# Kernel optimization log

Measured on AMD Instinct MI355X. Metric: run time of the kernel, lower is better.

## Reference

```python
import jax, jax.numpy as jnp
import numpy as np

CONF_THRESH = 0.01
TOP_K = 200        # per-class NMS candidate cap
NMS_THRESH = 0.45
KEEP_TOP_K = 200   # global per-image cap; also output K
TEMPERATURE = 1.0
V0, V1 = 0.1, 0.2  # variances


def _nms_keep(bxs, scs):
    """Greedy NMS over candidates sorted descending by score.
    bxs: [M,4] (x1,y1,x2,y2), scs: [M] (invalid slots have score -1).
    Returns keep mask [M] (bool). Matches torch nm_suppression: a box j is
    suppressed by kept box i iff NOT (IoU(i,j) <= thresh) (NaN IoU suppresses)."""
    x1, y1, x2, y2 = bxs[:, 0], bxs[:, 1], bxs[:, 2], bxs[:, 3]
    area = (x2 - x1) * (y2 - y1)
    xx1 = jnp.maximum(x1[:, None], x1[None, :])
    yy1 = jnp.maximum(y1[:, None], y1[None, :])
    xx2 = jnp.minimum(x2[:, None], x2[None, :])
    yy2 = jnp.minimum(y2[:, None], y2[None, :])
    inter = jnp.clip(xx2 - xx1, 0.0) * jnp.clip(yy2 - yy1, 0.0)
    union = area[None, :] - inter + area[:, None]  # row i: area[i] + area[j] - inter
    iou = inter / union  # [M,M]
    M = scs.shape[0]
    valid = scs > CONF_THRESH

    def step(active, i):
        k_i = active[i]                                  # kept iff still active (sorted desc)
        sup = k_i & jnp.logical_not(iou[i] <= NMS_THRESH)
        return active & jnp.logical_not(sup), k_i

    _, keep = jax.lax.scan(step, valid, jnp.arange(M))
    return keep


def _forward(loc_data, conf_data, dbox_list):
    B, N, C = conf_data.shape
    M, K = TOP_K, KEEP_TOP_K
    # --- box decode (SSD) ---
    db = dbox_list[None]                                   # [1,N,4]
    cxcy = db[..., :2] + loc_data[..., :2] * V0 * db[..., 2:]
    wh = db[..., 2:] * jnp.exp(loc_data[..., 2:] * V1)
    mins = cxcy - wh * 0.5
    boxes = jnp.clip(jnp.concatenate([mins, mins + wh], -1), 0.0, 1.0)  # [B,N,4]
    # --- class scores ---
    probs = jax.nn.softmax(conf_data / TEMPERATURE, axis=-1)
    sc = jnp.swapaxes(probs[..., 1:], 1, 2)                # [B,C-1,N] (skip background)
    masked = jnp.where(sc > CONF_THRESH, sc, -1.0)
    top_sc, top_idx = jax.lax.top_k(masked, M)             # [B,C-1,M] desc
    cand = jnp.take_along_axis(boxes[:, None], top_idx[..., None], axis=2)  # [B,C-1,M,4]
    # --- per-class greedy NMS ---
    keep = jax.vmap(jax.vmap(_nms_keep))(cand, top_sc)     # [B,C-1,M]
    kept_sc = jnp.where(keep, top_sc, 0.0)
    # --- global keep_top_k across classes (torch topk over concatenated dets) ---
    flat = kept_sc.reshape(B, -1)
    order = jnp.argsort(-flat, axis=1)
    rank = jnp.argsort(order, axis=1)                      # inverse permutation = desc rank
    keep_g = (flat > 0.0) & (rank < K)
    fin_sc = jnp.where(keep_g, flat, 0.0).reshape(B, C - 1, M)
    fin_bx = jnp.where(keep_g.reshape(B, C - 1, M)[..., None], cand, 0.0)
    # --- per-class compaction (stable desc sort keeps NMS order among survivors) ---
    ord2 = jnp.argsort(-fin_sc, axis=2)
    sc_out = jnp.take_along_axis(fin_sc, ord2, axis=2)[..., :K]
    bx_out = jnp.take_along_axis(fin_bx, ord2[..., None], axis=2)[..., :K, :]
    body = jnp.concatenate([sc_out[..., None], bx_out], axis=-1)  # [B,C-1,K,5]
    bg = jnp.zeros((B, 1, K, 5), body.dtype)               # class 0 (background) row stays 0
    return jnp.concatenate([bg, body], axis=1)             # [B,C,K,5]


def setup_inputs() -> dict:
    key = jax.random.key(0)
    k1, k2, k3 = jax.random.split(key, 3)
    B, N, C = 8, 32768, 81
    loc_data = jax.random.normal(k1, (B, N, 4), jnp.float32)
    conf_data = jax.random.normal(k2, (B, N, C), jnp.float32)
    dbox_list = jax.random.uniform(k3, (N, 4), jnp.float32, 0.05, 0.95)  # cx,cy,w,h priors
    return {"loc_data": loc_data, "conf_data": conf_data, "dbox_list": dbox_list}


def reference(loc_data, conf_data, dbox_list):
    return _forward(loc_data, conf_data, dbox_list)
```

## Files before the change

### kernel.cpp

```cpp
#include <hip/hip_runtime.h>
#include <stdint.h>

#define CONF_T 0.01f
#define NMS_T  0.45f
#define M_TOP  200
#define SM_ROWS 64
#define TK_BS  256
#define TCAP   4096

__device__ __forceinline__ uint32_t fkey(float f) {
    uint32_t u = __float_as_uint(f);
    return (u & 0x80000000u) ? ~u : (u | 0x80000000u);
}
__device__ __forceinline__ float fkey_inv(uint32_t k) {
    uint32_t u = (k & 0x80000000u) ? (k & 0x7FFFFFFFu) : ~k;
    return __uint_as_float(u);
}

__device__ __forceinline__ void suffix_select(
        uint32_t* hist, uint32_t* part, int nb, uint32_t pref, int shift,
        uint32_t wantv, uint32_t* s_prefix, uint32_t* s_want) {
    int tid = threadIdx.x;
    int bpt = nb >> 8;
    int base = tid * bpt;
    uint32_t loc = 0;
    for (int j = 0; j < bpt; j++) loc += hist[base + j];
    part[tid] = loc;
    __syncthreads();
    for (int d = 1; d < 256; d <<= 1) {
        uint32_t y = (tid + d < 256) ? part[tid + d] : 0u;
        __syncthreads();
        part[tid] += y;
        __syncthreads();
    }
    uint32_t run = part[tid] - loc;
    for (int j = bpt - 1; j >= 0; j--) {
        uint32_t h = hist[base + j];
        uint32_t sfx = run + h;
        if (run < wantv && sfx >= wantv) {
            *s_prefix = pref | ((uint32_t)(base + j) << shift);
            *s_want   = wantv - run;
        }
        run = sfx;
    }
    __syncthreads();
}

__device__ __forceinline__ float4 decode_box(float4 l, float4 d) {
    float cx = d.x + (l.x * 0.1f) * d.z;
    float cy = d.y + (l.y * 0.1f) * d.w;
    float w  = d.z * expf(l.z * 0.2f);
    float h  = d.w * expf(l.w * 0.2f);
    float x1 = cx - w * 0.5f, y1 = cy - h * 0.5f;
    float x2 = x1 + w, y2 = y1 + h;
    float4 o;
    o.x = fminf(fmaxf(x1, 0.f), 1.f);
    o.y = fminf(fmaxf(y1, 0.f), 1.f);
    o.z = fminf(fmaxf(x2, 0.f), 1.f);
    o.w = fminf(fmaxf(y2, 0.f), 1.f);
    return o;
}

__global__ __launch_bounds__(SM_ROWS) void softmax_kernel(
        const float* __restrict__ conf, float* __restrict__ sc,
        int B, int N, int C) {
    __shared__ float rows[SM_ROWS * 81];
    int tid = threadIdx.x;
    int BN = B * N;
    long long r0 = (long long)blockIdx.x * SM_ROWS;
    int nrows = BN - (int)r0; if (nrows > SM_ROWS) nrows = SM_ROWS;
    int totalf = nrows * 81;
    const float* g = conf + r0 * 81;
    int total4 = totalf >> 2;
    const float4* g4 = (const float4*)g;
    float4* l4 = (float4*)rows;
    for (int i = tid; i < total4; i += SM_ROWS) l4[i] = g4[i];
    for (int i = (total4 << 2) + tid; i < totalf; i += SM_ROWS) rows[i] = g[i];
    __syncthreads();
    if (tid < nrows) {
        float* p = rows + tid * 81;
        float m = p[0];
        for (int c = 1; c < 81; c++) m = fmaxf(m, p[c]);
        float s = 0.f;
        for (int c = 0; c < 81; c++) { float e = expf(p[c] - m); p[c] = e; s += e; }
        int r = (int)r0 + tid;
        int b = r / N, n = r % N;
        size_t base = ((size_t)b * (C - 1)) * N + n;
        for (int c = 1; c < 81; c++) {
            sc[base + (size_t)(c - 1) * N] = p[c] / s;
        }
    }
}

__global__ __launch_bounds__(TK_BS) void topk_kernel(
        const float* __restrict__ sc, const float* __restrict__ loc,
        const float* __restrict__ dbox,
        float* __restrict__ cand,
        float* __restrict__ cmpval, int* __restrict__ cmpidx,
        int* __restrict__ pcnt,
        int B, int N, int Cm1, int M) {
    const uint32_t KEYN1 = 0x407FFFFFu;
    const uint32_t BIN_N1 = KEYN1 >> 21;
    __shared__ uint32_t hist[2048];
    __shared__ uint32_t part[256];
    __shared__ uint32_t tk[TCAP];
    __shared__ int      tix[TCAP];
    __shared__ uint32_t s_prefix, s_want;
    __shared__ uint32_t ngt, ntie, tcnt;
    __shared__ float    e_val[256];
    __shared__ int      e_idx[256];
    __shared__ int      tiebuf[256];
    __shared__ float    s_sc[M_TOP];
    __shared__ float    s_x1[M_TOP], s_y1[M_TOP], s_x2[M_TOP], s_y2[M_TOP];

    int row = blockIdx.x;
    int b = row / Cm1, c = row % Cm1;
    int tid = threadIdx.x;
    const float* v = sc + (size_t)row * N;
    const float4* v4 = (const float4*)v;
    int n4 = N >> 2;

    bool sampled = (N >= 2048) && ((N & 7) == 0);
    uint32_t lo_key = 0xFFFFFFFFu, hi_key = 0xFFFFFFFFu;
    if (sampled) {
        int stride = N >> 3;
        for (int s = 0; s < 8; s++) {
            float f = v[s * stride + tid];
            tk[s * 256 + tid] = fkey(f > CONF_T ? f : -1.0f);
        }
        for (int i = tid; i < 2048; i += TK_BS) hist[i] = 0;
        __syncthreads();
        for (int i = tid; i < 2048; i += TK_BS) atomicAdd(&hist[tk[i] >> 21], 1u);
        __syncthreads();
        suffix_select(hist, part, 2048, 0u, 21, 3u, &s_prefix, &s_want);
        uint32_t h = s_prefix >> 21;
        suffix_select(hist, part, 2048, 0u, 21, 25u, &s_prefix, &s_want);
        uint32_t l = s_prefix >> 21;
        hi_key = ((h + 1) << 21) - 1u;
        lo_key = (l << 21) - 1u;
        sampled = (l > BIN_N1);
    }

    e_val[tid] = -1.0f; e_idx[tid] = tid;
    if (tid == 0) { ngt = 0; ntie = 0; tcnt = 0; }
    __syncthreads();

    bool ok = false;
    uint32_t G = 0, T = 0;
    if (sampled) {
        for (int i = tid; i < n4; i += TK_BS) {
            float4 f = v4[i];
            float mv[4] = { f.x > CONF_T ? f.x : -1.0f, f.y > CONF_T ? f.y : -1.0f,
                            f.z > CONF_T ? f.z : -1.0f, f.w > CONF_T ? f.w : -1.0f };
            #pragma unroll
            for (int j = 0; j < 4; j++) {
                uint32_t k = fkey(mv[j]);
                if (k > lo_key) {
                    int idx = 4 * i + j;
                    if (k > hi_key) {
                        uint32_t p = atomicAdd(&ngt, 1u);
                        if (p < 256) { e_val[p] = mv[j]; e_idx[p] = idx; }
                    } else {
                        uint32_t p = atomicAdd(&tcnt, 1u);
                        if (p < TCAP) { tk[p] = k; tix[p] = idx; }
                    }
                }
            }
        }
        for (int i = (n4 << 2) + tid; i < N; i += TK_BS) {
            float f = v[i];
            float mv = f > CONF_T ? f : -1.0f;
            uint32_t k = fkey(mv);
            if (k > lo_key) {
                if (k > hi_key) {
                    uint32_t p = atomicAdd(&ngt, 1u);
                    if (p < 256) { e_val[p] = mv; e_idx[p] = i; }
                } else {
                    uint32_t p = atomicAdd(&tcnt, 1u);
                    if (p < TCAP) { tk[p] = k; tix[p] = i; }
                }
            }
        }
        __syncthreads();
        G = ngt; T = tcnt;
        ok = (G <= (uint32_t)M_TOP) && (T <= (uint32_t)TCAP) &&
             (G + T >= (uint32_t)M_TOP);
    }

    uint32_t kth = KEYN1, rfin = 0;
    if (ok) {
        uint32_t want_t = (uint32_t)M_TOP - G;
        if (want_t > 0) {
            for (int i = tid; i < 2048; i += TK_BS) hist[i] = 0;
            __syncthreads();
            for (int i = tid; i < (int)T; i += TK_BS) atomicAdd(&hist[tk[i] >> 21], 1u);
            __syncthreads();
            suffix_select(hist, part, 2048, 0u, 21, want_t, &s_prefix, &s_want);
            uint32_t pre0 = s_prefix, w0 = s_want;
            uint32_t bb0 = pre0 >> 21;
            for (int i = tid; i < 2048; i += TK_BS) hist[i] = 0;
            __syncthreads();
            for (int i = tid; i < (int)T; i += TK_BS)
                if ((tk[i] >> 21) == bb0) atomicAdd(&hist[(tk[i] >> 10) & 2047u], 1u);
            __syncthreads();
            suffix_select(hist, part, 2048, pre0, 10, w0, &s_prefix, &s_want);
            uint32_t pre1 = s_prefix, w1 = s_want;
            for (int i = tid; i < 1024; i += TK_BS) hist[i] = 0;
            __syncthreads();
            for (int i = tid; i < (int)T; i += TK_BS)
                if ((tk[i] >> 10) == (pre1 >> 10)) atomicAdd(&hist[tk[i] & 1023u], 1u);
            __syncthreads();
            suffix_select(hist, part, 1024, pre1, 0, w1, &s_prefix, &s_want);
            kth = s_prefix; rfin = s_want;
            for (int i = tid; i < (int)T; i += TK_BS) {
                uint32_t k = tk[i];
                if (k > kth) {
                    uint32_t p = atomicAdd(&ngt, 1u);
                    if (p < 256) { e_val[p] = fkey_inv(k); e_idx[p] = tix[i]; }
                } else if (k == kth) {
                    uint32_t p = atomicAdd(&ntie, 1u);
                    if (p < 256) tiebuf[p] = tix[i];
                }
            }
            __syncthreads();
        }
    } else {
        e_val[tid] = -1.0f; e_idx[tid] = tid;
        if (tid == 0) { ngt = 0; ntie = 0; tcnt = 0; }
        for (int i = tid; i < 2048; i += TK_BS) hist[i] = 0;
        __syncthreads();
        for (int i = tid; i < n4; i += TK_BS) {
            float4 f = v4[i];
            atomicAdd(&hist[fkey(f.x > CONF_T ? f.x : -1.0f) >> 21], 1u);
            atomicAdd(&hist[fkey(f.y > CONF_T ? f.y : -1.0f) >> 21], 1u);
            atomicAdd(&hist[fkey(f.z > CONF_T ? f.z : -1.0f) >> 21], 1u);
            atomicAdd(&hist[fkey(f.w > CONF_T ? f.w : -1.0f) >> 21], 1u);
        }
        for (int i = (n4 << 2) + tid; i < N; i += TK_BS)
            atomicAdd(&hist[fkey(v[i] > CONF_T ? v[i] : -1.0f) >> 21], 1u);
        __syncthreads();
        suffix_select(hist, part, 2048, 0u, 21, M_TOP, &s_prefix, &s_want);
        uint32_t b0 = s_prefix >> 21;
        uint32_t want1 = s_want;
        bool collect_ties = (b0 != BIN_N1);
        for (int i = tid; i < N; i += TK_BS) {
            float f = v[i];
            float mv = f > CONF_T ? f : -1.0f;
            uint32_t k = fkey(mv);
            uint32_t bin = k >> 21;
            if (bin > b0) {
                uint32_t p = atomicAdd(&ngt, 1u);
                if (p < 256) { e_val[p] = mv; e_idx[p] = i; }
            } else if (bin == b0 && collect_ties) {
                uint32_t p = atomicAdd(&tcnt, 1u);
                if (p < TCAP) { tk[p] = k; tix[p] = i; }
            }
        }
        __syncthreads();
        if (collect_ties && tcnt <= TCAP) {
            int Tl = (int)tcnt;
            for (int i = tid; i < 2048; i += TK_BS) hist[i] = 0;
            __syncthreads();
            for (int i = tid; i < Tl; i += TK_BS) atomicAdd(&hist[(tk[i] >> 10) & 2047u], 1u);
            __syncthreads();
            suffix_select(hist, part, 2048, b0 << 21, 10, want1, &s_prefix, &s_want);
            uint32_t pre2 = s_prefix; uint32_t want2 = s_want;
            uint32_t b1 = (pre2 >> 10) & 2047u;
            for (int i = tid; i < 1024; i += TK_BS) hist[i] = 0;
            __syncthreads();
            for (int i = tid; i < Tl; i += TK_BS)
                if (((tk[i] >> 10) & 2047u) == b1) atomicAdd(&hist[tk[i] & 1023u], 1u);
            __syncthreads();
            suffix_select(hist, part, 1024, pre2, 0, want2, &s_prefix, &s_want);
            kth = s_prefix; rfin = s_want;
            for (int i = tid; i < Tl; i += TK_BS) {
                uint32_t k = tk[i];
                if (k > kth) {
                    uint32_t p = atomicAdd(&ngt, 1u);
                    if (p < 256) { e_val[p] = fkey_inv(k); e_idx[p] = tix[i]; }
                } else if (k == kth) {
                    uint32_t p = atomicAdd(&ntie, 1u);
                    if (p < 256) tiebuf[p] = tix[i];
                }
            }
            __syncthreads();
        } else if (collect_ties) {
            const int shifts[2] = {10, 0};
            const int nbins_[2] = {2048, 1024};
            if (tid == 0) { s_prefix = b0 << 21; s_want = want1; }
            __syncthreads();
            for (int lev = 0; lev < 2; lev++) {
                int shift = shifts[lev];
                int nb = nbins_[lev];
                uint32_t bmask = (uint32_t)nb - 1u;
                uint32_t pref = s_prefix, wantv = s_want;
                uint32_t pmask = 0xFFFFFFFFu << (shift + ((nb == 2048) ? 11 : 10));
                for (int i = tid; i < nb; i += TK_BS) hist[i] = 0;
                __syncthreads();
                for (int i = tid; i < N; i += TK_BS) {
                    float f = v[i];
                    uint32_t k = fkey(f > CONF_T ? f : -1.0f);
                    if ((k & pmask) == (pref & pmask)) atomicAdd(&hist[(k >> shift) & bmask], 1u);
                }
                __syncthreads();
                suffix_select(hist, part, nb, pref, shift, wantv, &s_prefix, &s_want);
            }
            kth = s_prefix; rfin = s_want;
            for (int i = tid; i < N; i += TK_BS) {
                float f = v[i];
                float mv = f > CONF_T ? f : -1.0f;
                uint32_t k = fkey(mv);
                if ((k >> 21) == b0) {
                    if (k > kth) {
                        uint32_t p = atomicAdd(&ngt, 1u);
                        if (p < 256) { e_val[p] = mv; e_idx[p] = i; }
                    } else if (k == kth) {
                        uint32_t p = atomicAdd(&ntie, 1u);
                        if (p < 256) tiebuf[p] = i;
                    }
                }
            }
            __syncthreads();
        }
    }

    uint32_t gcount = min(ngt, (uint32_t)M_TOP);
    uint32_t nt = min(ntie, 256u);
    if (tid < (int)nt) {
        int mine = tiebuf[tid];
        uint32_t rk = 0;
        for (uint32_t j = 0; j < nt; j++) if (tiebuf[j] < mine) rk++;
        if (rk < rfin) {
            uint32_t slot = gcount + rk;
            if (slot < M_TOP) { e_val[slot] = fkey_inv(kth); e_idx[slot] = mine; }
        }
    }
    __syncthreads();
    if (tid < M_TOP) {
        float mv = e_val[tid]; int mi = e_idx[tid];
        uint32_t mk = fkey(mv);
        uint32_t rk = 0;
        for (int j = 0; j < M_TOP; j++) {
            uint32_t jk = fkey(e_val[j]); int ji = e_idx[j];
            if (jk > mk || (jk == mk && ji < mi)) rk++;
        }
        float4 l = ((const float4*)loc)[(size_t)b * N + mi];
        float4 d = ((const float4*)dbox)[mi];
        float4 bx = decode_box(l, d);
        ((float4*)cand)[(size_t)row * M_TOP + rk] = bx;
        s_sc[rk] = mv;
        s_x1[rk] = bx.x; s_y1[rk] = bx.y; s_x2[rk] = bx.z; s_y2[rk] = bx.w;
    }
    __syncthreads();

    if (tid < 64) {
        int lane = tid;
        float x1[4], y1[4], x2[4], y2[4], ar[4], sv[4];
        int act[4], kf[4];
        #pragma unroll
        for (int s = 0; s < 4; s++) {
            int j = s * 64 + lane;
            if (j < M_TOP) {
                x1[s] = s_x1[j]; y1[s] = s_y1[j]; x2[s] = s_x2[j]; y2[s] = s_y2[j];
                ar[s] = (x2[s] - x1[s]) * (y2[s] - y1[s]);
                sv[s] = s_sc[j];
            } else { x1[s]=0.f; y1[s]=0.f; x2[s]=0.f; y2[s]=0.f; ar[s]=0.f; sv[s]=-1.0f; }
            act[s] = (sv[s] > CONF_T) ? 1 : 0;
            kf[s] = 0;
        }
        #pragma unroll
        for (int si = 0; si < 4; si++) {
            int lim = M_TOP - si * 64; if (lim > 64) lim = 64;
            for (int li = 0; li < lim; li++) {
                int a = __shfl(act[si], li);
                if (a) {
                    if (lane == li) kf[si] = 1;
                    float bx1 = __shfl(x1[si], li);
                    float by1 = __shfl(y1[si], li);
                    float bx2 = __shfl(x2[si], li);
                    float by2 = __shfl(y2[si], li);
                    float bar = __shfl(ar[si], li);
                    #pragma unroll
                    for (int s = 0; s < 4; s++) {
                        float xx1 = fmaxf(bx1, x1[s]);
                        float yy1 = fmaxf(by1, y1[s]);
                        float xx2 = fminf(bx2, x2[s]);
                        float yy2 = fminf(by2, y2[s]);
                        float inter = fmaxf(xx2 - xx1, 0.f) * fmaxf(yy2 - yy1, 0.f);
                        float uni = (ar[s] - inter) + bar;
                        float iou = inter / uni;
                        if (!(iou <= NMS_T)) act[s] = 0;
                    }
                }
            }
        }
        unsigned long long ball[4];
        int total = 0;
        #pragma unroll
        for (int s = 0; s < 4; s++) { ball[s] = __ballot(kf[s] != 0); total += (int)__popcll(ball[s]); }
        int base = 0;
        if (lane == 0 && total > 0) base = atomicAdd(&pcnt[b], total);
        base = __shfl(base, 0);
        unsigned long long lower = (lane == 0) ? 0ull : (~0ull >> (64 - lane));
        int off = base;
        #pragma unroll
        for (int s = 0; s < 4; s++) {
            if (kf[s]) {
                int pos = off + (int)__popcll(ball[s] & lower);
                cmpval[(size_t)b * M + pos] = sv[s];
                cmpidx[(size_t)b * M + pos] = c * M_TOP + s * 64 + lane;
            }
            off += (int)__popcll(ball[s]);
        }
    }
}

__global__ __launch_bounds__(256) void gtop_kernel(
        const float* __restrict__ cmpval, const int* __restrict__ cmpidx,
        const int* __restrict__ pcnt, float* __restrict__ gl_val,
        int* __restrict__ gl_idx, int* __restrict__ gl_cnt, int M) {
    int b = blockIdx.x;
    int tid = threadIdx.x;
    int P = pcnt[b];
    const float* cv = cmpval + (size_t)b * M;
    const int*   ci = cmpidx + (size_t)b * M;
    if (P <= M_TOP) {
        for (int i = tid; i < P; i += 256) {
            gl_val[b * M_TOP + i] = cv[i];
            gl_idx[b * M_TOP + i] = ci[i];
        }
        if (tid == 0) gl_cnt[b] = P;
        return;
    }
    __shared__ uint32_t hist[256];
    __shared__ uint32_t s_prefix, s_want;
    __shared__ int tiebuf[256];
    __shared__ uint32_t ntie, wcnt;
    __shared__ int cutoff;
    if (tid == 0) { s_prefix = 0; s_want = M_TOP; }
    for (int pass = 0; pass < 4; pass++) {
        hist[tid] = 0;
        __syncthreads();
        uint32_t prefix = s_prefix;
        int shift = 24 - 8 * pass;
        for (int i = tid; i < P; i += 256) {
            uint32_t k = fkey(cv[i]);
            bool ok = (pass == 0) || ((k >> (shift + 8)) == (prefix >> (shift + 8)));
            if (ok) atomicAdd(&hist[(k >> shift) & 255u], 1u);
        }
        __syncthreads();
        if (tid == 0) {
            uint32_t want = s_want, cum = 0; int bin = 0;
            for (int bb = 255; bb >= 0; bb--) {
                if (cum + hist[bb] >= want) { bin = bb; break; }
                cum += hist[bb];
            }
            s_want = want - cum;
            s_prefix = prefix | ((uint32_t)bin << shift);
        }
        __syncthreads();
    }
    uint32_t kth = s_prefix, rfin = s_want;
    if (tid == 0) { ntie = 0; cutoff = -1; wcnt = 0; }
    __syncthreads();
    for (int i = tid; i < P; i += 256) {
        if (fkey(cv[i]) == kth) { uint32_t p = atomicAdd(&ntie, 1u); if (p < 256) tiebuf[p] = ci[i]; }
    }
    __syncthreads();
    uint32_t nt = min(ntie, 256u);
    if (tid < (int)nt) {
        int mine = tiebuf[tid];
        uint32_t rk = 0;
        for (uint32_t j = 0; j < nt; j++) if (tiebuf[j] < mine) rk++;
        if (rk == rfin - 1) cutoff = mine;
    }
    __syncthreads();
    int cut = cutoff;
    for (int i = tid; i < P; i += 256) {
        uint32_t k = fkey(cv[i]);
        if (k > kth || (k == kth && ci[i] <= cut)) {
            uint32_t p = atomicAdd(&wcnt, 1u);
            gl_val[b * M_TOP + p] = cv[i];
            gl_idx[b * M_TOP + p] = ci[i];
        }
    }
    if (tid == 0) gl_cnt[b] = M_TOP;
}

__global__ __launch_bounds__(256) void out_kernel(
        const float* __restrict__ gl_val, const int* __restrict__ gl_idx,
        const int* __restrict__ gl_cnt, const float* __restrict__ cand,
        float* __restrict__ out, int C, int Cm1) {
    int row = blockIdx.x;
    int b = row / C, cc = row % C;
    int tid = threadIdx.x;
    size_t oslab = (size_t)row * M_TOP * 5;
    if (cc == 0) {
        for (int i = tid; i < M_TOP * 5; i += 256) out[oslab + i] = 0.0f;
        return;
    }
    int c = cc - 1;
    __shared__ float lv[M_TOP];
    __shared__ int   lm[M_TOP];
    __shared__ uint32_t nloc;
    if (tid == 0) nloc = 0;
    __syncthreads();
    int cnt = gl_cnt[b];
    for (int i = tid; i < cnt; i += 256) {
        int idx = gl_idx[b * M_TOP + i];
        if (idx / M_TOP == c) {
            uint32_t p = atomicAdd(&nloc, 1u);
            lv[p] = gl_val[b * M_TOP + i];
            lm[p] = idx % M_TOP;
        }
    }
    __syncthreads();
    int nc = (int)nloc;
    if (tid < M_TOP) {
        if (tid < nc) {
            float v = lv[tid]; int m = lm[tid];
            int rk = 0;
            for (int j = 0; j < nc; j++)
                if (lv[j] > v || (lv[j] == v && lm[j] < m)) rk++;
            float4 bb = ((const float4*)cand)[((size_t)(b * Cm1 + c)) * M_TOP + m];
            size_t o = oslab + (size_t)rk * 5;
            out[o] = v; out[o + 1] = bb.x; out[o + 2] = bb.y;
            out[o + 3] = bb.z; out[o + 4] = bb.w;
        } else {
            size_t o = oslab + (size_t)tid * 5;
            out[o] = 0.f; out[o + 1] = 0.f; out[o + 2] = 0.f;
            out[o + 3] = 0.f; out[o + 4] = 0.f;
        }
    }
}

extern "C" void kernel_launch(void* const* d_in, const int* in_sizes, int n_in,
                              void* d_out, int out_size, void* d_ws, size_t ws_size,
                              hipStream_t stream) {
    const float* loc  = (const float*)d_in[0];
    const float* conf = (const float*)d_in[1];
    const float* dbox = (const float*)d_in[2];
    int N   = in_sizes[2] / 4;
    int B   = in_sizes[0] / (4 * N);
    int C   = in_sizes[1] / (B * N);
    int Cm1 = C - 1;
    int M   = Cm1 * M_TOP;

    char* ws = (char*)d_ws;
    size_t off = 0;
    auto alloc = [&](size_t bytes) -> char* {
        char* p = ws + off;
        off = (off + bytes + 255) & ~(size_t)255;
        return p;
    };
    float* sc     = (float*)alloc((size_t)B * Cm1 * N * sizeof(float));
    float* cand   = (float*)alloc((size_t)B * M * 4 * sizeof(float));
    int*   pcnt   = (int*)alloc((size_t)B * sizeof(int));
    float* cmpval = (float*)alloc((size_t)B * M * sizeof(float));
    int*   cmpidx = (int*)alloc((size_t)B * M * sizeof(int));
    float* gl_val = (float*)alloc((size_t)B * M_TOP * sizeof(float));
    int*   gl_idx = (int*)alloc((size_t)B * M_TOP * sizeof(int));
    int*   gl_cnt = (int*)alloc((size_t)B * sizeof(int));

    int bn = B * N;
    hipMemsetAsync(pcnt, 0, (size_t)B * sizeof(int), stream);
    softmax_kernel<<<(bn + SM_ROWS - 1) / SM_ROWS, SM_ROWS, 0, stream>>>(conf, sc, B, N, C);
    topk_kernel<<<B * Cm1, TK_BS, 0, stream>>>(sc, loc, dbox, cand, cmpval, cmpidx, pcnt,
                                               B, N, Cm1, M);
    gtop_kernel<<<B, 256, 0, stream>>>(cmpval, cmpidx, pcnt, gl_val, gl_idx, gl_cnt, M);
    out_kernel<<<B * C, 256, 0, stream>>>(gl_val, gl_idx, gl_cnt, cand, (float*)d_out, C, Cm1);
}
```

Measured before the change: 335.4 us.

## Precompute NMS IoU bitmask matrix in parallel and use wave-shuffle suffix scans

The per-class NMS now has 200 threads each build a 200-bit suppression mask in shared memory, reusing the tk buffer. A single wave then runs the greedy pass with only 64-bit shuffles and mask ANDs, instead of recomputing IoUs with divisions at every step. The histogram suffix scan in suffix_select drops the shared-memory Hillis-Steele loop, which had many block barriers, for wave-level shuffle scans plus a 4-entry cross-wave sum. Output compaction moves to a block-wide pass driven by the shared keep masks. The cost is extra shared-memory traffic, an extra pass of barriers, and O(M²) IoU work done up front even for boxes that end up suppressed.

```diff
diff --git a/kernel.cpp b/kernel.cpp
--- a/kernel.cpp
+++ b/kernel.cpp
@@ -18,30 +18,33 @@
 }
 
 __device__ __forceinline__ void suffix_select(
-        uint32_t* hist, uint32_t* part, int nb, uint32_t pref, int shift,
+        uint32_t* hist, uint32_t* wsum, int nb, uint32_t pref, int shift,
         uint32_t wantv, uint32_t* s_prefix, uint32_t* s_want) {
     int tid = threadIdx.x;
+    int lane = tid & 63, w = tid >> 6;
     int bpt = nb >> 8;
     int base = tid * bpt;
     uint32_t loc = 0;
     for (int j = 0; j < bpt; j++) loc += hist[base + j];
-    part[tid] = loc;
-    __syncthreads();
-    for (int d = 1; d < 256; d <<= 1) {
-        uint32_t y = (tid + d < 256) ? part[tid + d] : 0u;
-        __syncthreads();
-        part[tid] += y;
-        __syncthreads();
-    }
-    uint32_t run = part[tid] - loc;
+    uint32_t sfx = loc;
+    #pragma unroll
+    for (int d = 1; d < 64; d <<= 1) {
+        uint32_t y = __shfl_down(sfx, d);
+        if (lane + d < 64) sfx += y;
+    }
+    if (lane == 0) wsum[w] = sfx;
+    __syncthreads();
+    uint32_t later = 0;
+    for (int j = w + 1; j < TK_BS / 64; j++) later += wsum[j];
+    uint32_t run = (sfx - loc) + later;
     for (int j = bpt - 1; j >= 0; j--) {
         uint32_t h = hist[base + j];
-        uint32_t sfx = run + h;
-        if (run < wantv && sfx >= wantv) {
+        uint32_t s2 = run + h;
+        if (run < wantv && s2 >= wantv) {
             *s_prefix = pref | ((uint32_t)(base + j) << shift);
             *s_want   = wantv - run;
         }
-        run = sfx;
+        run = s2;
     }
     __syncthreads();
 }
@@ -101,17 +104,19 @@
         int B, int N, int Cm1, int M) {
     const uint32_t KEYN1 = 0x407FFFFFu;
     const uint32_t BIN_N1 = KEYN1 >> 21;
-    __shared__ uint32_t hist[2048];
-    __shared__ uint32_t part[256];
-    __shared__ uint32_t tk[TCAP];
+    __shared__ __align__(16) uint32_t hist[2048];
+    __shared__ __align__(16) uint32_t tk[TCAP];
     __shared__ int      tix[TCAP];
+    __shared__ uint32_t wsum[TK_BS / 64];
     __shared__ uint32_t s_prefix, s_want;
     __shared__ uint32_t ngt, ntie, tcnt;
     __shared__ float    e_val[256];
     __shared__ int      e_idx[256];
     __shared__ int      tiebuf[256];
     __shared__ float    s_sc[M_TOP];
-    __shared__ float    s_x1[M_TOP], s_y1[M_TOP], s_x2[M_TOP], s_y2[M_TOP];
+    __shared__ float    s_x1[M_TOP], s_y1[M_TOP], s_x2[M_TOP], s_y2[M_TOP], s_ar[M_TOP];
+    __shared__ unsigned long long s_keep[4];
+    __shared__ int s_base;
 
     int row = blockIdx.x;
     int b = row / Cm1, c = row % Cm1;
@@ -132,9 +137,9 @@
         __syncthreads();
         for (int i = tid; i < 2048; i += TK_BS) atomicAdd(&hist[tk[i] >> 21], 1u);
         __syncthreads();
-        suffix_select(hist, part, 2048, 0u, 21, 3u, &s_prefix, &s_want);
+        suffix_select(hist, wsum, 2048, 0u, 21, 3u, &s_prefix, &s_want);
         uint32_t h = s_prefix >> 21;
-        suffix_select(hist, part, 2048, 0u, 21, 25u, &s_prefix, &s_want);
+        suffix_select(hist, wsum, 2048, 0u, 21, 25u, &s_prefix, &s_want);
         uint32_t l = s_prefix >> 21;
         hi_key = ((h + 1) << 21) - 1u;
         lo_key = (l << 21) - 1u;
@@ -195,7 +200,7 @@
             __syncthreads();
             for (int i = tid; i < (int)T; i += TK_BS) atomicAdd(&hist[tk[i] >> 21], 1u);
             __syncthreads();
-            suffix_select(hist, part, 2048, 0u, 21, want_t, &s_prefix, &s_want);
+            suffix_select(hist, wsum, 2048, 0u, 21, want_t, &s_prefix, &s_want);
             uint32_t pre0 = s_prefix, w0 = s_want;
             uint32_t bb0 = pre0 >> 21;
             for (int i = tid; i < 2048; i += TK_BS) hist[i] = 0;
@@ -203,14 +208,14 @@
             for (int i = tid; i < (int)T; i += TK_BS)
                 if ((tk[i] >> 21) == bb0) atomicAdd(&hist[(tk[i] >> 10) & 2047u], 1u);
             __syncthreads();
-            suffix_select(hist, part, 2048, pre0, 10, w0, &s_prefix, &s_want);
+            suffix_select(hist, wsum, 2048, pre0, 10, w0, &s_prefix, &s_want);
             uint32_t pre1 = s_prefix, w1 = s_want;
             for (int i = tid; i < 1024; i += TK_BS) hist[i] = 0;
             __syncthreads();
             for (int i = tid; i < (int)T; i += TK_BS)
                 if ((tk[i] >> 10) == (pre1 >> 10)) atomicAdd(&hist[tk[i] & 1023u], 1u);
             __syncthreads();
-            suffix_select(hist, part, 1024, pre1, 0, w1, &s_prefix, &s_want);
+            suffix_select(hist, wsum, 1024, pre1, 0, w1, &s_prefix, &s_want);
             kth = s_prefix; rfin = s_want;
             for (int i = tid; i < (int)T; i += TK_BS) {
                 uint32_t k = tk[i];
@@ -239,7 +244,7 @@
         for (int i = (n4 << 2) + tid; i < N; i += TK_BS)
             atomicAdd(&hist[fkey(v[i] > CONF_T ? v[i] : -1.0f) >> 21], 1u);
         __syncthreads();
-        suffix_select(hist, part, 2048, 0u, 21, M_TOP, &s_prefix, &s_want);
+        suffix_select(hist, wsum, 2048, 0u, 21, M_TOP, &s_prefix, &s_want);
         uint32_t b0 = s_prefix >> 21;
         uint32_t want1 = s_want;
         bool collect_ties = (b0 != BIN_N1);
@@ -263,7 +268,7 @@
             __syncthreads();
             for (int i = tid; i < Tl; i += TK_BS) atomicAdd(&hist[(tk[i] >> 10) & 2047u], 1u);
             __syncthreads();
-            suffix_select(hist, part, 2048, b0 << 21, 10, want1, &s_prefix, &s_want);
+            suffix_select(hist, wsum, 2048, b0 << 21, 10, want1, &s_prefix, &s_want);
             uint32_t pre2 = s_prefix; uint32_t want2 = s_want;
             uint32_t b1 = (pre2 >> 10) & 2047u;
             for (int i = tid; i < 1024; i += TK_BS) hist[i] = 0;
@@ -271,7 +276,7 @@
             for (int i = tid; i < Tl; i += TK_BS)
                 if (((tk[i] >> 10) & 2047u) == b1) atomicAdd(&hist[tk[i] & 1023u], 1u);
             __syncthreads();
-            suffix_select(hist, part, 1024, pre2, 0, want2, &s_prefix, &s_want);
+            suffix_select(hist, wsum, 1024, pre2, 0, want2, &s_prefix, &s_want);
             kth = s_prefix; rfin = s_want;
             for (int i = tid; i < Tl; i += TK_BS) {
                 uint32_t k = tk[i];
@@ -303,7 +308,7 @@
                     if ((k & pmask) == (pref & pmask)) atomicAdd(&hist[(k >> shift) & bmask], 1u);
                 }
                 __syncthreads();
-                suffix_select(hist, part, nb, pref, shift, wantv, &s_prefix, &s_want);
+                suffix_select(hist, wsum, nb, pref, shift, wantv, &s_prefix, &s_want);
             }
             kth = s_prefix; rfin = s_want;
             for (int i = tid; i < N; i += TK_BS) {
@@ -353,64 +358,73 @@
     }
     __syncthreads();
 
+    unsigned long long* sup = (unsigned long long*)tk;
+    if (tid < M_TOP) s_ar[tid] = (s_x2[tid] - s_x1[tid]) * (s_y2[tid] - s_y1[tid]);
+    __syncthreads();
+    if (tid < M_TOP) {
+        float ix1 = s_x1[tid], iy1 = s_y1[tid], ix2 = s_x2[tid], iy2 = s_y2[tid];
+        float iar = s_ar[tid];
+        unsigned long long m[4] = {0ull, 0ull, 0ull, 0ull};
+        for (int j = 0; j < M_TOP; j++) {
+            float xx1 = fmaxf(ix1, s_x1[j]);
+            float yy1 = fmaxf(iy1, s_y1[j]);
+            float xx2 = fminf(ix2, s_x2[j]);
+            float yy2 = fminf(iy2, s_y2[j]);
+            float inter = fmaxf(xx2 - xx1, 0.f) * fmaxf(yy2 - yy1, 0.f);
+            float uni = (s_ar[j] - inter) + iar;
+            float iou = inter / uni;
+            if (!(iou <= NMS_T)) m[j >> 6] |= 1ull << (j & 63);
+        }
+        sup[tid * 4 + 0] = m[0]; sup[tid * 4 + 1] = m[1];
+        sup[tid * 4 + 2] = m[2]; sup[tid * 4 + 3] = m[3];
+    }
+    __syncthreads();
     if (tid < 64) {
         int lane = tid;
-        float x1[4], y1[4], x2[4], y2[4], ar[4], sv[4];
-        int act[4], kf[4];
+        unsigned long long r0[4], r1[4], r2[4], r3[4];
+        #pragma unroll
+        for (int k = 0; k < 4; k++) {
+            r0[k] = sup[lane * 4 + k];
+            r1[k] = sup[(64 + lane) * 4 + k];
+            r2[k] = sup[(128 + lane) * 4 + k];
+            r3[k] = (192 + lane < M_TOP) ? sup[(192 + lane) * 4 + k] : 0ull;
+        }
+        unsigned long long act[4];
         #pragma unroll
         for (int s = 0; s < 4; s++) {
             int j = s * 64 + lane;
-            if (j < M_TOP) {
-                x1[s] = s_x1[j]; y1[s] = s_y1[j]; x2[s] = s_x2[j]; y2[s] = s_y2[j];
-                ar[s] = (x2[s] - x1[s]) * (y2[s] - y1[s]);
-                sv[s] = s_sc[j];
-            } else { x1[s]=0.f; y1[s]=0.f; x2[s]=0.f; y2[s]=0.f; ar[s]=0.f; sv[s]=-1.0f; }
-            act[s] = (sv[s] > CONF_T) ? 1 : 0;
-            kf[s] = 0;
-        }
-        #pragma unroll
-        for (int si = 0; si < 4; si++) {
-            int lim = M_TOP - si * 64; if (lim > 64) lim = 64;
-            for (int li = 0; li < lim; li++) {
-                int a = __shfl(act[si], li);
-                if (a) {
-                    if (lane == li) kf[si] = 1;
-                    float bx1 = __shfl(x1[si], li);
-                    float by1 = __shfl(y1[si], li);
-                    float bx2 = __shfl(x2[si], li);
-                    float by2 = __shfl(y2[si], li);
-                    float bar = __shfl(ar[si], li);
-                    #pragma unroll
-                    for (int s = 0; s < 4; s++) {
-                        float xx1 = fmaxf(bx1, x1[s]);
-                        float yy1 = fmaxf(by1, y1[s]);
-                        float xx2 = fminf(bx2, x2[s]);
-                        float yy2 = fminf(by2, y2[s]);
-                        float inter = fmaxf(xx2 - xx1, 0.f) * fmaxf(yy2 - yy1, 0.f);
-                        float uni = (ar[s] - inter) + bar;
-                        float iou = inter / uni;
-                        if (!(iou <= NMS_T)) act[s] = 0;
-                    }
-                }
-            }
-        }
-        unsigned long long ball[4];
-        int total = 0;
-        #pragma unroll
-        for (int s = 0; s < 4; s++) { ball[s] = __ballot(kf[s] != 0); total += (int)__popcll(ball[s]); }
-        int base = 0;
-        if (lane == 0 && total > 0) base = atomicAdd(&pcnt[b], total);
-        base = __shfl(base, 0);
-        unsigned long long lower = (lane == 0) ? 0ull : (~0ull >> (64 - lane));
-        int off = base;
-        #pragma unroll
-        for (int s = 0; s < 4; s++) {
-            if (kf[s]) {
-                int pos = off + (int)__popcll(ball[s] & lower);
-                cmpval[(size_t)b * M + pos] = sv[s];
-                cmpidx[(size_t)b * M + pos] = c * M_TOP + s * 64 + lane;
-            }
-            off += (int)__popcll(ball[s]);
+            bool a = (j < M_TOP) && (s_sc[j] > CONF_T);
+            act[s] = __ballot(a);
+        }
+        unsigned long long keep[4] = {0ull, 0ull, 0ull, 0ull};
+        for (int i = 0; i < M_TOP; i++) {
+            int w = i >> 6, b2 = i & 63;
+            if ((act[w] >> b2) & 1ull) {
+                keep[w] |= 1ull << b2;
+                unsigned long long m0, m1, m2, m3;
+                if (w == 0)      { m0 = __shfl(r0[0], b2); m1 = __shfl(r0[1], b2); m2 = __shfl(r0[2], b2); m3 = __shfl(r0[3], b2); }
+                else if (w == 1) { m0 = __shfl(r1[0], b2); m1 = __shfl(r1[1], b2); m2 = __shfl(r1[2], b2); m3 = __shfl(r1[3], b2); }
+                else if (w == 2) { m0 = __shfl(r2[0], b2); m1 = __shfl(r2[1], b2); m2 = __shfl(r2[2], b2); m3 = __shfl(r2[3], b2); }
+                else             { m0 = __shfl(r3[0], b2); m1 = __shfl(r3[1], b2); m2 = __shfl(r3[2], b2); m3 = __shfl(r3[3], b2); }
+                act[0] &= ~m0; act[1] &= ~m1; act[2] &= ~m2; act[3] &= ~m3;
+            }
+        }
+        if (lane < 4) s_keep[lane] = keep[lane];
+        if (lane == 0) {
+            int total = __popcll(keep[0]) + __popcll(keep[1]) +
+                        __popcll(keep[2]) + __popcll(keep[3]);
+            s_base = (total > 0) ? atomicAdd(&pcnt[b], total) : 0;
+        }
+    }
+    __syncthreads();
+    if (tid < M_TOP) {
+        unsigned long long kw = s_keep[tid >> 6];
+        if ((kw >> (tid & 63)) & 1ull) {
+            int pos = s_base;
+            for (int w = 0; w < (tid >> 6); w++) pos += __popcll(s_keep[w]);
+            pos += __popcll(kw & ((1ull << (tid & 63)) - 1ull));
+            cmpval[(size_t)b * M + pos] = s_sc[tid];
+            cmpidx[(size_t)b * M + pos] = c * M_TOP + tid;
         }
     }
 }
```

Result: slower. 371.0 us (+10.6%).

## Rewrite softmax to register-per-row loads and use wave-shuffle suffix scan

Applied to the files above, without the earlier changes.

The softmax kernel drops the shared-memory staging of 64 rows and instead has each of 256 threads load its own 81-float row into registers through unaligned float4 loads, then write the transposed scores directly. The suffix_select block scan replaces a shared-memory Hillis-Steele scan that needs many barriers with a wave-level shuffle scan plus a small per-wave sum array. The softmax change trades coalesced global reads for strided per-thread row reads and more register pressure, though the larger blocks may raise occupancy.

```diff
diff --git a/kernel.cpp b/kernel.cpp
--- a/kernel.cpp
+++ b/kernel.cpp
@@ -4,9 +4,10 @@
 #define CONF_T 0.01f
 #define NMS_T  0.45f
 #define M_TOP  200
-#define SM_ROWS 64
 #define TK_BS  256
 #define TCAP   4096
+
+typedef float float4u __attribute__((ext_vector_type(4), aligned(4)));
 
 __device__ __forceinline__ uint32_t fkey(float f) {
     uint32_t u = __float_as_uint(f);
@@ -18,30 +19,33 @@
 }
 
 __device__ __forceinline__ void suffix_select(
-        uint32_t* hist, uint32_t* part, int nb, uint32_t pref, int shift,
+        uint32_t* hist, uint32_t* wsum, int nb, uint32_t pref, int shift,
         uint32_t wantv, uint32_t* s_prefix, uint32_t* s_want) {
     int tid = threadIdx.x;
+    int lane = tid & 63, w = tid >> 6;
     int bpt = nb >> 8;
     int base = tid * bpt;
     uint32_t loc = 0;
     for (int j = 0; j < bpt; j++) loc += hist[base + j];
-    part[tid] = loc;
-    __syncthreads();
-    for (int d = 1; d < 256; d <<= 1) {
-        uint32_t y = (tid + d < 256) ? part[tid + d] : 0u;
-        __syncthreads();
-        part[tid] += y;
-        __syncthreads();
-    }
-    uint32_t run = part[tid] - loc;
+    uint32_t sfx = loc;
+    #pragma unroll
+    for (int d = 1; d < 64; d <<= 1) {
+        uint32_t y = __shfl_down(sfx, d);
+        if (lane + d < 64) sfx += y;
+    }
+    if (lane == 0) wsum[w] = sfx;
+    __syncthreads();
+    uint32_t later = 0;
+    for (int j = w + 1; j < TK_BS / 64; j++) later += wsum[j];
+    uint32_t run = (sfx - loc) + later;
     for (int j = bpt - 1; j >= 0; j--) {
         uint32_t h = hist[base + j];
-        uint32_t sfx = run + h;
-        if (run < wantv && sfx >= wantv) {
+        uint32_t s2 = run + h;
+        if (run < wantv && s2 >= wantv) {
             *s_prefix = pref | ((uint32_t)(base + j) << shift);
             *s_want   = wantv - run;
         }
-        run = sfx;
+        run = s2;
     }
     __syncthreads();
 }
@@ -61,35 +65,29 @@
     return o;
 }
 
-__global__ __launch_bounds__(SM_ROWS) void softmax_kernel(
+__global__ __launch_bounds__(256, 4) void softmax_kernel(
         const float* __restrict__ conf, float* __restrict__ sc,
         int B, int N, int C) {
-    __shared__ float rows[SM_ROWS * 81];
-    int tid = threadIdx.x;
-    int BN = B * N;
-    long long r0 = (long long)blockIdx.x * SM_ROWS;
-    int nrows = BN - (int)r0; if (nrows > SM_ROWS) nrows = SM_ROWS;
-    int totalf = nrows * 81;
-    const float* g = conf + r0 * 81;
-    int total4 = totalf >> 2;
-    const float4* g4 = (const float4*)g;
-    float4* l4 = (float4*)rows;
-    for (int i = tid; i < total4; i += SM_ROWS) l4[i] = g4[i];
-    for (int i = (total4 << 2) + tid; i < totalf; i += SM_ROWS) rows[i] = g[i];
-    __syncthreads();
-    if (tid < nrows) {
-        float* p = rows + tid * 81;
-        float m = p[0];
-        for (int c = 1; c < 81; c++) m = fmaxf(m, p[c]);
-        float s = 0.f;
-        for (int c = 0; c < 81; c++) { float e = expf(p[c] - m); p[c] = e; s += e; }
-        int r = (int)r0 + tid;
-        int b = r / N, n = r % N;
-        size_t base = ((size_t)b * (C - 1)) * N + n;
-        for (int c = 1; c < 81; c++) {
-            sc[base + (size_t)(c - 1) * N] = p[c] / s;
-        }
-    }
+    int r = blockIdx.x * blockDim.x + threadIdx.x;
+    if (r >= B * N) return;
+    const float* p = conf + (size_t)r * 81;
+    float v[81];
+    #pragma unroll
+    for (int i = 0; i < 20; i++) {
+        float4u f = *(const float4u*)(p + 4 * i);
+        v[4 * i] = f.x; v[4 * i + 1] = f.y; v[4 * i + 2] = f.z; v[4 * i + 3] = f.w;
+    }
+    v[80] = p[80];
+    float m = v[0];
+    #pragma unroll
+    for (int c = 1; c < 81; c++) m = fmaxf(m, v[c]);
+    float s = 0.f;
+    #pragma unroll
+    for (int c = 0; c < 81; c++) { float e = expf(v[c] - m); v[c] = e; s += e; }
+    int b = r / N, n = r % N;
+    float* obase = sc + ((size_t)b * (C - 1)) * N + n;
+    #pragma unroll
+    for (int c = 1; c < 81; c++) obase[(size_t)(c - 1) * N] = v[c] / s;
 }
 
 __global__ __launch_bounds__(TK_BS) void topk_kernel(
@@ -101,10 +99,10 @@
         int B, int N, int Cm1, int M) {
     const uint32_t KEYN1 = 0x407FFFFFu;
     const uint32_t BIN_N1 = KEYN1 >> 21;
-    __shared__ uint32_t hist[2048];
-    __shared__ uint32_t part[256];
-    __shared__ uint32_t tk[TCAP];
+    __shared__ __align__(16) uint32_t hist[2048];
+    __shared__ __align__(16) uint32_t tk[TCAP];
     __shared__ int      tix[TCAP];
+    __shared__ uint32_t wsum[TK_BS / 64];
     __shared__ uint32_t s_prefix, s_want;
     __shared__ uint32_t ngt, ntie, tcnt;
     __shared__ float    e_val[256];
@@ -132,9 +130,9 @@
         __syncthreads();
         for (int i = tid; i < 2048; i += TK_BS) atomicAdd(&hist[tk[i] >> 21], 1u);
         __syncthreads();
-        suffix_select(hist, part, 2048, 0u, 21, 3u, &s_prefix, &s_want);
+        suffix_select(hist, wsum, 2048, 0u, 21, 3u, &s_prefix, &s_want);
         uint32_t h = s_prefix >> 21;
-        suffix_select(hist, part, 2048, 0u, 21, 25u, &s_prefix, &s_want);
+        suffix_select(hist, wsum, 2048, 0u, 21, 25u, &s_prefix, &s_want);
         uint32_t l = s_prefix >> 21;
         hi_key = ((h + 1) << 21) - 1u;
         lo_key = (l << 21) - 1u;
@@ -195,7 +193,7 @@
             __syncthreads();
             for (int i = tid; i < (int)T; i += TK_BS) atomicAdd(&hist[tk[i] >> 21], 1u);
             __syncthreads();
-            suffix_select(hist, part, 2048, 0u, 21, want_t, &s_prefix, &s_want);
+            suffix_select(hist, wsum, 2048, 0u, 21, want_t, &s_prefix, &s_want);
             uint32_t pre0 = s_prefix, w0 = s_want;
             uint32_t bb0 = pre0 >> 21;
             for (int i = tid; i < 2048; i += TK_BS) hist[i] = 0;
@@ -203,14 +201,14 @@
             for (int i = tid; i < (int)T; i += TK_BS)
                 if ((tk[i] >> 21) == bb0) atomicAdd(&hist[(tk[i] >> 10) & 2047u], 1u);
             __syncthreads();
-            suffix_select(hist, part, 2048, pre0, 10, w0, &s_prefix, &s_want);
+            suffix_select(hist, wsum, 2048, pre0, 10, w0, &s_prefix, &s_want);
             uint32_t pre1 = s_prefix, w1 = s_want;
             for (int i = tid; i < 1024; i += TK_BS) hist[i] = 0;
             __syncthreads();
             for (int i = tid; i < (int)T; i += TK_BS)
                 if ((tk[i] >> 10) == (pre1 >> 10)) atomicAdd(&hist[tk[i] & 1023u], 1u);
             __syncthreads();
-            suffix_select(hist, part, 1024, pre1, 0, w1, &s_prefix, &s_want);
+            suffix_select(hist, wsum, 1024, pre1, 0, w1, &s_prefix, &s_want);
             kth = s_prefix; rfin = s_want;
             for (int i = tid; i < (int)T; i += TK_BS) {
                 uint32_t k = tk[i];
@@ -239,7 +237,7 @@
         for (int i = (n4 << 2) + tid; i < N; i += TK_BS)
             atomicAdd(&hist[fkey(v[i] > CONF_T ? v[i] : -1.0f) >> 21], 1u);
         __syncthreads();
-        suffix_select(hist, part, 2048, 0u, 21, M_TOP, &s_prefix, &s_want);
+        suffix_select(hist, wsum, 2048, 0u, 21, M_TOP, &s_prefix, &s_want);
         uint32_t b0 = s_prefix >> 21;
         uint32_t want1 = s_want;
         bool collect_ties = (b0 != BIN_N1);
@@ -263,7 +261,7 @@
             __syncthreads();
             for (int i = tid; i < Tl; i += TK_BS) atomicAdd(&hist[(tk[i] >> 10) & 2047u], 1u);
             __syncthreads();
-            suffix_select(hist, part, 2048, b0 << 21, 10, want1, &s_prefix, &s_want);
+            suffix_select(hist, wsum, 2048, b0 << 21, 10, want1, &s_prefix, &s_want);
             uint32_t pre2 = s_prefix; uint32_t want2 = s_want;
             uint32_t b1 = (pre2 >> 10) & 2047u;
             for (int i = tid; i < 1024; i += TK_BS) hist[i] = 0;
@@ -271,7 +269,7 @@
             for (int i = tid; i < Tl; i += TK_BS)
                 if (((tk[i] >> 10) & 2047u) == b1) atomicAdd(&hist[tk[i] & 1023u], 1u);
             __syncthreads();
-            suffix_select(hist, part, 1024, pre2, 0, want2, &s_prefix, &s_want);
+            suffix_select(hist, wsum, 1024, pre2, 0, want2, &s_prefix, &s_want);
             kth = s_prefix; rfin = s_want;
             for (int i = tid; i < Tl; i += TK_BS) {
                 uint32_t k = tk[i];
@@ -303,7 +301,7 @@
                     if ((k & pmask) == (pref & pmask)) atomicAdd(&hist[(k >> shift) & bmask], 1u);
                 }
                 __syncthreads();
-                suffix_select(hist, part, nb, pref, shift, wantv, &s_prefix, &s_want);
+                suffix_select(hist, wsum, nb, pref, shift, wantv, &s_prefix, &s_want);
             }
             kth = s_prefix; rfin = s_want;
             for (int i = tid; i < N; i += TK_BS) {
@@ -564,7 +562,7 @@
 
     int bn = B * N;
     hipMemsetAsync(pcnt, 0, (size_t)B * sizeof(int), stream);
-    softmax_kernel<<<(bn + SM_ROWS - 1) / SM_ROWS, SM_ROWS, 0, stream>>>(conf, sc, B, N, C);
+    softmax_kernel<<<(bn + 255) / 256, 256, 0, stream>>>(conf, sc, B, N, C);
     topk_kernel<<<B * Cm1, TK_BS, 0, stream>>>(sc, loc, dbox, cand, cmpval, cmpidx, pcnt,
                                                B, N, Cm1, M);
     gtop_kernel<<<B, 256, 0, stream>>>(cmpval, cmpidx, pcnt, gl_val, gl_idx, gl_cnt, M);
```

New measurement: 299.9 us. -10.6%, faster.
